# Optimization experiments

Hardware: AMD Instinct MI355X
Metric: run time of the kernel (lower is better)

## Reference

```python
import jax, jax.numpy as jnp
import numpy as np

DIM = 256; SEQ = 2048; WIN = 64; HEADS = 4; RANK = 32; LAYERS = 3; VOCAB = 32000
EPS = 1e-6

def _unit(v):
    # unit_normalize_values: project onto unit sphere along feature dim
    return v / jnp.maximum(jnp.linalg.norm(v, axis=-1, keepdims=True), EPS)

def _signed_softmax(s):
    # signed_softmax_state: sign(s) * softmax(|s|) over nodes
    return jnp.sign(s) * jax.nn.softmax(jnp.abs(s), axis=-1)

def setup_inputs() -> dict:
    key = jax.random.key(0)
    ks = jax.random.split(key, 10)
    d = DIM
    return {
        "input_ids": jax.random.randint(ks[0], (2, SEQ), 0, VOCAB, dtype=jnp.int32),
        "emb": 0.02 * jax.random.normal(ks[1], (VOCAB, d), jnp.float32),
        "pos_emb": 0.02 * jax.random.normal(ks[2], (SEQ, d), jnp.float32),
        "anchor_val": 0.02 * jax.random.normal(ks[3], (d,), jnp.float32),
        "anchor_state": jnp.zeros((), jnp.float32),
        "Ws": 0.02 * jax.random.normal(ks[4], (d,), jnp.float32),
        "bs": jnp.zeros((), jnp.float32),
        "U": 0.02 * jax.random.normal(ks[5], (LAYERS, d, HEADS, RANK), jnp.float32),
        "V": 0.02 * jax.random.normal(ks[6], (LAYERS, d, HEADS, RANK), jnp.float32),
        "W1": 0.02 * jax.random.normal(ks[7], (LAYERS, d, 2 * d), jnp.float32),
        "b1": jnp.zeros((LAYERS, 2 * d), jnp.float32),
        "W2": 0.02 * jax.random.normal(ks[8], (LAYERS, 2 * d, d), jnp.float32),
        "b2": jnp.zeros((LAYERS, d), jnp.float32),
    }

def _forward(emb, pos_emb, anchor_val, anchor_state, Ws, bs, U, V, W1, b1, W2, b2, input_ids):
    B, S = input_ids.shape
    tok = emb[input_ids] + pos_emb[None, :S]          # [B,S,D]
    state_src = tok                                    # state projected from pre-unit-norm values
    tok = _unit(tok)
    tstate = state_src @ Ws + bs                       # [B,S] scalar state per node
    val = jnp.concatenate([jnp.broadcast_to(_unit(anchor_val), (B, 1, DIM)), tok], axis=1)
    state = jnp.concatenate([jnp.broadcast_to(anchor_state, (B, 1)), tstate], axis=1)
    N = S + 1
    offs = jnp.arange(-WIN, WIN + 1)
    idx = jnp.arange(N)[:, None] + offs[None, :]       # [N,K]
    valid = (idx >= 0) & (idx < N)
    idxc = jnp.clip(idx, 0, N - 1)
    inv_sqrt_r = np.float32(1.0 / np.sqrt(RANK))
    for l in range(LAYERS):
        q = jnp.einsum('bnd,dhr->bnhr', val, U[l])
        k = jnp.einsum('bnd,dhr->bnhr', val, V[l])
        knb = k[:, idxc]                               # [B,N,K,H,R] window gather
        s = jnp.einsum('bnhr,bnkhr->bnkh', q, knb) * inv_sqrt_r
        s = s.max(axis=-1)                             # max head-aggregate [B,N,K]
        a = jnp.where(valid, jnp.abs(s), -jnp.inf)
        wgt = jnp.where(valid, jnp.sign(s) * jax.nn.softmax(a, axis=-1), 0.0)  # signed-abs-softmax edges
        dval = jnp.einsum('bnk,bnkd->bnd', wgt, val[:, idxc])
        dstate = jnp.sum(wgt * state[:, idxc], axis=-1)
        # apply_delta: residual + norm(identity) + unit-norm + touched-mask where
        updated = val + dval
        nv = _unit(updated)
        touched = jnp.max(jnp.abs(jax.lax.stop_gradient(dval)), axis=-1, keepdims=True) > 0
        val = jnp.where(touched, nv, updated)
        state = _signed_softmax(state + dstate)
        # residual feed-forward then re-unit-norm
        h = jax.nn.gelu(jnp.einsum('bnd,dh->bnh', val, W1[l]) + b1[l], approximate=False)
        val = _unit(val + jnp.einsum('bnh,hd->bnd', h, W2[l]) + b2[l])
    return state, val

def reference(input_ids, emb, pos_emb, anchor_val, anchor_state, Ws, bs, U, V, W1, b1, W2, b2):
    return _forward(emb, pos_emb, anchor_val, anchor_state, Ws, bs, U, V, W1, b1, W2, b2, input_ids)
```

## Files before the change

kernel.cpp:

```cpp
#include <hip/hip_runtime.h>
#include <hip/hip_bf16.h>
#include <math.h>

#define BB 2
#define SS 2048
#define NN 2049
#define MM (BB*NN)
#define DD 256
#define HR 128
#define NHEAD 4
#define WINW 64
#define DFF 512
#define EPSF 1e-6f
#define TB8 257

typedef __attribute__((ext_vector_type(8))) short bf16x8;
typedef __attribute__((ext_vector_type(4))) float f32x4;

__device__ __forceinline__ float wave_sum(float v) {
    v += __shfl_down(v, 32, 64); v += __shfl_down(v, 16, 64);
    v += __shfl_down(v, 8, 64);  v += __shfl_down(v, 4, 64);
    v += __shfl_down(v, 2, 64);  v += __shfl_down(v, 1, 64);
    return v;
}
__device__ __forceinline__ float wave_max(float v) {
    v = fmaxf(v, __shfl_down(v, 32, 64)); v = fmaxf(v, __shfl_down(v, 16, 64));
    v = fmaxf(v, __shfl_down(v, 8, 64));  v = fmaxf(v, __shfl_down(v, 4, 64));
    v = fmaxf(v, __shfl_down(v, 2, 64));  v = fmaxf(v, __shfl_down(v, 1, 64));
    return v;
}
__device__ __forceinline__ float block_sum(float v, float* red) {
    v = wave_sum(v);
    __syncthreads();
    if ((threadIdx.x & 63) == 0) red[threadIdx.x >> 6] = v;
    __syncthreads();
    return red[0] + red[1] + red[2] + red[3];
}
__device__ __forceinline__ float sgnf(float x) {
    return (x > 0.f) ? 1.f : ((x < 0.f) ? -1.f : 0.f);
}
__device__ __forceinline__ ushort f2b(float x) {
    __hip_bfloat16 h = __float2bfloat16(x);
    return *(ushort*)&h;
}
__device__ __forceinline__ float b2f(ushort u) {
    unsigned int v = ((unsigned int)u) << 16;
    return *(float*)&v;
}
__device__ __forceinline__ void split3(float x, ushort& h, ushort& m, ushort& l) {
    h = f2b(x);
    float r1 = x - b2f(h);
    m = f2b(r1);
    l = f2b(r1 - b2f(m));
}
__device__ __forceinline__ void pack_map(int e, int N, int& k, int& n) {
    int j = e & 7;
    int l = (e >> 3) & 63;
    int c = e >> 9;
    int ntiles = N >> 4;
    int kt = c / ntiles, nt = c - kt * ntiles;
    k = kt * 32 + ((l >> 4) << 3) + j;
    n = nt * 16 + (l & 15);
}

__global__ void pre_kernel(const int* __restrict__ ids,
                           const float* __restrict__ emb,
                           const float* __restrict__ pos,
                           const float* __restrict__ anchor_val,
                           const float* __restrict__ anchor_state,
                           const float* __restrict__ Ws,
                           const float* __restrict__ bs,
                           float* __restrict__ val,
                           float* __restrict__ state,
                           const float* __restrict__ W1, const float* __restrict__ W2,
                           const float* __restrict__ U,  const float* __restrict__ V,
                           ushort* __restrict__ W1ph, ushort* __restrict__ W1pl,
                           ushort* __restrict__ W2ph, ushort* __restrict__ W2pl,
                           ushort* __restrict__ U0, ushort* __restrict__ U1,
                           ushort* __restrict__ U2,
                           ushort* __restrict__ V0, ushort* __restrict__ V1,
                           ushort* __restrict__ V2) {
    __shared__ float red[4];
    int bid = blockIdx.x;
    int t = threadIdx.x;
    if (bid < MM) {
        int b = bid / NN, n = bid % NN;
        float e;
        if (n == 0) {
            e = anchor_val[t];
        } else {
            int id = ids[b * SS + (n - 1)];
            e = emb[(size_t)id * DD + t] + pos[(size_t)(n - 1) * DD + t];
        }
        float ss = block_sum(e * e, red);
        float ts = block_sum(e * Ws[t], red);
        float rn = 1.f / fmaxf(sqrtf(ss), EPSF);
        float o = e * rn;
        val[(size_t)bid * DD + t] = o;
        if (t == 0) state[bid] = (n == 0) ? anchor_state[0] : (ts + bs[0]);
        return;
    }
    int idx = (bid - MM) * 256 + t;
    int l = idx / 327680;
    int r = idx - l * 327680;
    if (l >= 3) return;
    int k, n;
    if (r < 131072) {
        int e = r;
        pack_map(e, 512, k, n);
        float s = W1[(size_t)l * 131072 + (size_t)k * 512 + n];
        ushort h = f2b(s);
        W1ph[(size_t)l * 131072 + e] = h;
        W1pl[(size_t)l * 131072 + e] = f2b(s - b2f(h));
    } else if (r < 262144) {
        int e = r - 131072;
        pack_map(e, 256, k, n);
        float s = W2[(size_t)l * 131072 + (size_t)k * 256 + n];
        ushort h = f2b(s);
        W2ph[(size_t)l * 131072 + e] = h;
        W2pl[(size_t)l * 131072 + e] = f2b(s - b2f(h));
    } else if (r < 294912) {
        int e = r - 262144;
        pack_map(e, 128, k, n);
        ushort h, m, lo;
        split3(U[(size_t)l * 32768 + (size_t)k * 128 + n], h, m, lo);
        U0[(size_t)l * 32768 + e] = h;
        U1[(size_t)l * 32768 + e] = m;
        U2[(size_t)l * 32768 + e] = lo;
    } else {
        int e = r - 294912;
        pack_map(e, 128, k, n);
        ushort h, m, lo;
        split3(V[(size_t)l * 32768 + (size_t)k * 128 + n], h, m, lo);
        V0[(size_t)l * 32768 + e] = h;
        V1[(size_t)l * 32768 + e] = m;
        V2[(size_t)l * 32768 + e] = lo;
    }
}

__global__ __launch_bounds__(256, 3)
void proj_kernel(const float* __restrict__ Xin,
                 const ushort* __restrict__ U0, const ushort* __restrict__ U1,
                 const ushort* __restrict__ U2,
                 const ushort* __restrict__ V0, const ushort* __restrict__ V1,
                 const ushort* __restrict__ V2,
                 ushort* __restrict__ q0, ushort* __restrict__ q1,
                 ushort* __restrict__ q2,
                 ushort* __restrict__ k0, ushort* __restrict__ k1,
                 ushort* __restrict__ k2,
                 float* __restrict__ valG, int donorm) {
    __shared__ __align__(16) ushort pln[3][16 * 256];
    int t = threadIdx.x;
    int w = t >> 6, l = t & 63;
    int lm = l & 15, quad = l >> 4;
    int m0 = blockIdx.x * 16;
    bool isQ = (blockIdx.y == 0);
    const ushort* P0 = isQ ? U0 : V0;
    const ushort* P1 = isQ ? U1 : V1;
    const ushort* P2 = isQ ? U2 : V2;

    #pragma unroll
    for (int rr = 0; rr < 4; rr++) {
        int row = w * 4 + rr;
        int tok = m0 + row; if (tok > MM - 1) tok = MM - 1;
        f32x4 x = *(const f32x4*)(Xin + (size_t)tok * DD + l * 4);
        if (donorm) {
            float s = x[0]*x[0] + x[1]*x[1] + x[2]*x[2] + x[3]*x[3];
            #pragma unroll
            for (int off = 1; off < 64; off <<= 1) s += __shfl_xor(s, off, 64);
            float rn = 1.f / fmaxf(sqrtf(s), EPSF);
            x[0] *= rn; x[1] *= rn; x[2] *= rn; x[3] *= rn;
            if (isQ) *(f32x4*)(valG + (size_t)tok * DD + l * 4) = x;
        }
        ushort4 h4, m4, l4;
        ushort hh, mm, ll;
        split3(x[0], hh, mm, ll); h4.x = hh; m4.x = mm; l4.x = ll;
        split3(x[1], hh, mm, ll); h4.y = hh; m4.y = mm; l4.y = ll;
        split3(x[2], hh, mm, ll); h4.z = hh; m4.z = mm; l4.z = ll;
        split3(x[3], hh, mm, ll); h4.w = hh; m4.w = mm; l4.w = ll;
        unsigned byte = ((unsigned)(row * 512 + l * 8)) ^ ((unsigned)((row & 7) << 4));
        *(ushort4*)((char*)&pln[0][0] + byte) = h4;
        *(ushort4*)((char*)&pln[1][0] + byte) = m4;
        *(ushort4*)((char*)&pln[2][0] + byte) = l4;
    }
    __syncthreads();

    f32x4 acc[2];
    acc[0] = (f32x4)(0.f); acc[1] = (f32x4)(0.f);
    #pragma unroll
    for (int kt = 0; kt < 8; kt++) {
        unsigned abyte = ((unsigned)(lm * 512 + kt * 64 + quad * 16)) ^
                         ((unsigned)((lm & 7) << 4));
        bf16x8 a0 = *(const bf16x8*)((char*)&pln[0][0] + abyte);
        bf16x8 a1 = *(const bf16x8*)((char*)&pln[1][0] + abyte);
        bf16x8 a2 = *(const bf16x8*)((char*)&pln[2][0] + abyte);
        #pragma unroll
        for (int jj = 0; jj < 2; jj++) {
            int ntl = w * 2 + jj;
            size_t off = ((size_t)(kt * 8 + ntl) * 64 + l) * 8;
            bf16x8 b0 = *(const bf16x8*)(P0 + off);
            bf16x8 b1 = *(const bf16x8*)(P1 + off);
            bf16x8 b2 = *(const bf16x8*)(P2 + off);
            acc[jj] = __builtin_amdgcn_mfma_f32_16x16x32_bf16(a0, b0, acc[jj], 0, 0, 0);
            acc[jj] = __builtin_amdgcn_mfma_f32_16x16x32_bf16(a0, b1, acc[jj], 0, 0, 0);
            acc[jj] = __builtin_amdgcn_mfma_f32_16x16x32_bf16(a1, b0, acc[jj], 0, 0, 0);
            acc[jj] = __builtin_amdgcn_mfma_f32_16x16x32_bf16(a1, b1, acc[jj], 0, 0, 0);
            acc[jj] = __builtin_amdgcn_mfma_f32_16x16x32_bf16(a0, b2, acc[jj], 0, 0, 0);
            acc[jj] = __builtin_amdgcn_mfma_f32_16x16x32_bf16(a2, b0, acc[jj], 0, 0, 0);
        }
    }
    ushort* o0 = isQ ? q0 : k0;
    ushort* o1 = isQ ? q1 : k1;
    ushort* o2 = isQ ? q2 : k2;
    #pragma unroll
    for (int jj = 0; jj < 2; jj++) {
        int n = (w * 2 + jj) * 16 + lm;
        #pragma unroll
        for (int r = 0; r < 4; r++) {
            int tok = m0 + quad * 4 + r;
            if (tok < MM) {
                ushort h, m, lo;
                split3(acc[jj][r], h, m, lo);
                size_t oi = (size_t)tok * HR + n;
                o0[oi] = h; o1[oi] = m; o2[oi] = lo;
            }
        }
    }
}

__global__ __launch_bounds__(256, 3)
void attn_kernel(const float* __restrict__ val_in,
                 const float* __restrict__ state_in,
                 const ushort* __restrict__ q0, const ushort* __restrict__ q1,
                 const ushort* __restrict__ q2,
                 const ushort* __restrict__ k0, const ushort* __restrict__ k1,
                 const ushort* __restrict__ k2,
                 float* __restrict__ val_out,
                 ushort* __restrict__ vbH, ushort* __restrict__ vbM,
                 float* __restrict__ dstate_out) {
    __shared__ float sc4[NHEAD][8][148];
    __shared__ float wgt2[144][12];
    __shared__ float redS[8][4];
    __shared__ float redM[8][4];

    int b = blockIdx.x / TB8;
    int n0 = (blockIdx.x % TB8) * 8;
    int t = threadIdx.x;
    int w = t >> 6, l = t & 63;
    int lm = l & 15, quad = l >> 4;

    {
        int qrow = n0 + (lm & 7);
        if (qrow > NN - 1) qrow = NN - 1;
        size_t qa = ((size_t)(b * NN + qrow)) * HR + w * 32 + quad * 8;
        bf16x8 a0 = *(const bf16x8*)(q0 + qa);
        bf16x8 a1 = *(const bf16x8*)(q1 + qa);
        bf16x8 a2 = *(const bf16x8*)(q2 + qa);
        #pragma unroll
        for (int jt = 0; jt < 9; jt++) {
            int j = n0 - 64 + jt * 16 + lm;
            j = (j < 0) ? 0 : ((j > NN - 1) ? NN - 1 : j);
            size_t ka = ((size_t)(b * NN + j)) * HR + w * 32 + quad * 8;
            bf16x8 kf0 = *(const bf16x8*)(k0 + ka);
            bf16x8 kf1 = *(const bf16x8*)(k1 + ka);
            bf16x8 kf2 = *(const bf16x8*)(k2 + ka);
            f32x4 acc = (f32x4)(0.f);
            acc = __builtin_amdgcn_mfma_f32_16x16x32_bf16(a0, kf0, acc, 0, 0, 0);
            acc = __builtin_amdgcn_mfma_f32_16x16x32_bf16(a0, kf1, acc, 0, 0, 0);
            acc = __builtin_amdgcn_mfma_f32_16x16x32_bf16(a1, kf0, acc, 0, 0, 0);
            acc = __builtin_amdgcn_mfma_f32_16x16x32_bf16(a1, kf1, acc, 0, 0, 0);
            acc = __builtin_amdgcn_mfma_f32_16x16x32_bf16(a0, kf2, acc, 0, 0, 0);
            acc = __builtin_amdgcn_mfma_f32_16x16x32_bf16(a2, kf0, acc, 0, 0, 0);
            if (quad < 2) {
                #pragma unroll
                for (int r = 0; r < 4; r++)
                    sc4[w][quad * 4 + r][jt * 16 + lm] = acc[r];
            }
        }
    }
    __syncthreads();

    {
        int m = t >> 5, p = t & 31;
        int n = n0 + m;
        bool tokv = (n < NN);
        float sv[5]; bool vv[5];
        float mx = -INFINITY;
        #pragma unroll
        for (int i = 0; i < 5; i++) {
            int tap = p + 32 * i;
            bool inb = (tap < 144);
            int tapc = inb ? tap : 0;
            int j = n0 - 64 + tapc;
            float s0 = sc4[0][m][tapc], s1 = sc4[1][m][tapc];
            float s2 = sc4[2][m][tapc], s3 = sc4[3][m][tapc];
            float s = fmaxf(fmaxf(s0, s1), fmaxf(s2, s3)) * 0.17677669529663687f;
            bool v = inb && tokv && (tap >= m) && (tap <= m + 128) && (j >= 0) && (j < NN);
            sv[i] = s; vv[i] = v;
            if (v) mx = fmaxf(mx, fabsf(s));
        }
        for (int off = 16; off > 0; off >>= 1) mx = fmaxf(mx, __shfl_xor(mx, off, 64));
        float ee[5];
        float sum = 0.f;
        #pragma unroll
        for (int i = 0; i < 5; i++) {
            ee[i] = vv[i] ? expf(fabsf(sv[i]) - mx) : 0.f;
            sum += ee[i];
        }
        for (int off = 16; off > 0; off >>= 1) sum += __shfl_xor(sum, off, 64);
        float inv = (sum > 0.f) ? 1.f / sum : 0.f;
        float ds = 0.f;
        #pragma unroll
        for (int i = 0; i < 5; i++) {
            int tap = p + 32 * i;
            if (tap < 144) {
                float wg = vv[i] ? sgnf(sv[i]) * ee[i] * inv : 0.f;
                wgt2[tap][m] = wg;
                if (vv[i]) ds += wg * state_in[b * NN + (n0 - 64 + tap)];
            }
        }
        for (int off = 16; off > 0; off >>= 1) ds += __shfl_xor(ds, off, 64);
        if (p == 0 && tokv) dstate_out[b * NN + n] = ds;
    }
    __syncthreads();

    {
        int d = (t >> 2) * 4;
        int tg = t & 3;
        int tok0 = tg * 2, tok1 = tg * 2 + 1;
        int jlo = (n0 >= 64) ? 0 : (64 - n0);
        int jhi = NN - 1 - n0 + 64; if (jhi > 135) jhi = 135;
        const float* vbase = val_in + ((size_t)(b * NN + n0 - 64)) * DD + d;
        f32x4 acc0 = (f32x4)(0.f), acc1 = (f32x4)(0.f);
        int jj = jlo;
        for (; jj + 3 <= jhi; jj += 4) {
            f32x4 v0 = *(const f32x4*)(vbase + (size_t)(jj + 0) * DD);
            f32x4 v1 = *(const f32x4*)(vbase + (size_t)(jj + 1) * DD);
            f32x4 v2 = *(const f32x4*)(vbase + (size_t)(jj + 2) * DD);
            f32x4 v3 = *(const f32x4*)(vbase + (size_t)(jj + 3) * DD);
            float wa0 = wgt2[jj + 0][tok0], wa1 = wgt2[jj + 0][tok1];
            float wb0 = wgt2[jj + 1][tok0], wb1 = wgt2[jj + 1][tok1];
            float wc0 = wgt2[jj + 2][tok0], wc1 = wgt2[jj + 2][tok1];
            float wd0 = wgt2[jj + 3][tok0], wd1 = wgt2[jj + 3][tok1];
            #pragma unroll
            for (int c = 0; c < 4; c++) {
                acc0[c] += v0[c] * wa0 + v1[c] * wb0 + v2[c] * wc0 + v3[c] * wd0;
                acc1[c] += v0[c] * wa1 + v1[c] * wb1 + v2[c] * wc1 + v3[c] * wd1;
            }
        }
        for (; jj <= jhi; jj++) {
            f32x4 v = *(const f32x4*)(vbase + (size_t)jj * DD);
            float w0 = wgt2[jj][tok0], w1 = wgt2[jj][tok1];
            #pragma unroll
            for (int c = 0; c < 4; c++) {
                acc0[c] += v[c] * w0;
                acc1[c] += v[c] * w1;
            }
        }
        f32x4 u[2]; f32x4 ac[2]; ac[0] = acc0; ac[1] = acc1;
        #pragma unroll
        for (int ti = 0; ti < 2; ti++) {
            int tok = tg * 2 + ti;
            int n = n0 + tok;
            f32x4 vold = (f32x4)(0.f);
            if (n < NN) vold = *(const f32x4*)(val_in + ((size_t)(b * NN + n)) * DD + d);
            u[ti] = vold + ac[ti];
            float s = u[ti][0]*u[ti][0] + u[ti][1]*u[ti][1] + u[ti][2]*u[ti][2] + u[ti][3]*u[ti][3];
            float mb = fmaxf(fmaxf(fabsf(ac[ti][0]), fabsf(ac[ti][1])),
                             fmaxf(fabsf(ac[ti][2]), fabsf(ac[ti][3])));
            for (int off = 4; off <= 32; off <<= 1) {
                s += __shfl_xor(s, off, 64);
                mb = fmaxf(mb, __shfl_xor(mb, off, 64));
            }
            if ((l >> 2) == 0) { redS[tok][w] = s; redM[tok][w] = mb; }
        }
        __syncthreads();
        #pragma unroll
        for (int ti = 0; ti < 2; ti++) {
            int tok = tg * 2 + ti;
            int n = n0 + tok;
            if (n < NN) {
                float ss = redS[tok][0] + redS[tok][1] + redS[tok][2] + redS[tok][3];
                float mab = fmaxf(fmaxf(redM[tok][0], redM[tok][1]),
                                  fmaxf(redM[tok][2], redM[tok][3]));
                float rn = 1.f / fmaxf(sqrtf(ss), EPSF);
                f32x4 o = u[ti];
                if (mab > 0.f) { o[0] *= rn; o[1] *= rn; o[2] *= rn; o[3] *= rn; }
                size_t oi = ((size_t)(b * NN + n)) * DD + d;
                *(f32x4*)(val_out + oi) = o;
                ushort4 hv, mv;
                {
                    ushort h0 = f2b(o[0]); hv.x = h0; mv.x = f2b(o[0] - b2f(h0));
                    ushort h1 = f2b(o[1]); hv.y = h1; mv.y = f2b(o[1] - b2f(h1));
                    ushort h2 = f2b(o[2]); hv.z = h2; mv.z = f2b(o[2] - b2f(h2));
                    ushort h3 = f2b(o[3]); hv.w = h3; mv.w = f2b(o[3] - b2f(h3));
                }
                *(ushort4*)(vbH + oi) = hv;
                *(ushort4*)(vbM + oi) = mv;
            }
        }
    }
}

__global__ __launch_bounds__(256, 3)
void ffn1_kernel(const ushort* __restrict__ XbH, const ushort* __restrict__ XbM,
                 const ushort* __restrict__ W1h, const ushort* __restrict__ W1l,
                 const float*  __restrict__ b1,
                 ushort* __restrict__ Hh, ushort* __restrict__ Hl,
                 const float* __restrict__ state_in, const float* __restrict__ dstate,
                 float* __restrict__ state_out) {
    __shared__ float red[8];
    int t = threadIdx.x;

    if (blockIdx.x == 257) {
        int b = blockIdx.y;
        float lmax = -INFINITY;
        for (int n = t; n < NN; n += 256) {
            float x = state_in[b * NN + n] + dstate[b * NN + n];
            lmax = fmaxf(lmax, fabsf(x));
        }
        lmax = wave_max(lmax);
        if ((t & 63) == 0) red[t >> 6] = lmax;
        __syncthreads();
        float m = fmaxf(fmaxf(red[0], red[1]), fmaxf(red[2], red[3]));
        float lsum = 0.f;
        for (int n = t; n < NN; n += 256)
            lsum += expf(fabsf(state_in[b * NN + n] + dstate[b * NN + n]) - m);
        lsum = wave_sum(lsum);
        __syncthreads();
        if ((t & 63) == 0) red[4 + (t >> 6)] = lsum;
        __syncthreads();
        float inv = 1.f / (red[4] + red[5] + red[6] + red[7]);
        for (int n = t; n < NN; n += 256) {
            float x = state_in[b * NN + n] + dstate[b * NN + n];
            state_out[b * NN + n] = sgnf(x) * expf(fabsf(x) - m) * inv;
        }
        return;
    }

    int w = t >> 6, l = t & 63;
    int lm = l & 15, quad = l >> 4;
    int m0 = blockIdx.x * 16;
    int nh = blockIdx.y;
    int row0 = m0 + lm; if (row0 > MM - 1) row0 = MM - 1;
    const ushort* xh = XbH + (size_t)row0 * DD + quad * 8;
    const ushort* xm = XbM + (size_t)row0 * DD + quad * 8;

    f32x4 acc[4];
    #pragma unroll
    for (int jj = 0; jj < 4; jj++) acc[jj] = (f32x4)(0.f);

    #pragma unroll
    for (int kt = 0; kt < 8; kt++) {
        bf16x8 ah = *(const bf16x8*)(xh + kt * 32);
        bf16x8 am = *(const bf16x8*)(xm + kt * 32);
        #pragma unroll
        for (int jj = 0; jj < 4; jj++) {
            int ntl = w * 4 + jj;
            size_t off = ((size_t)(kt * 32 + nh * 16 + ntl) * 64 + l) * 8;
            bf16x8 bh = *(const bf16x8*)(W1h + off);
            bf16x8 bl = *(const bf16x8*)(W1l + off);
            acc[jj] = __builtin_amdgcn_mfma_f32_16x16x32_bf16(ah, bh, acc[jj], 0, 0, 0);
            acc[jj] = __builtin_amdgcn_mfma_f32_16x16x32_bf16(am, bh, acc[jj], 0, 0, 0);
            acc[jj] = __builtin_amdgcn_mfma_f32_16x16x32_bf16(ah, bl, acc[jj], 0, 0, 0);
        }
    }
    #pragma unroll
    for (int jj = 0; jj < 4; jj++) {
        int gn = nh * 256 + (w * 4 + jj) * 16 + lm;
        float bb = b1[gn];
        #pragma unroll
        for (int r = 0; r < 4; r++) {
            int tok = m0 + quad * 4 + r;
            if (tok < MM) {
                float x = acc[jj][r] + bb;
                float g = 0.5f * x * (1.f + erff(x * 0.70710678118654752f));
                ushort gh = f2b(g);
                size_t oi = (size_t)tok * DFF + gn;
                Hh[oi] = gh;
                Hl[oi] = f2b(g - b2f(gh));
            }
        }
    }
}

__global__ __launch_bounds__(256, 4)
void ffn2_kernel(const ushort* __restrict__ Hh, const ushort* __restrict__ Hl,
                 const float*  __restrict__ Xf,
                 const ushort* __restrict__ W2h, const ushort* __restrict__ W2l,
                 const float*  __restrict__ b2,
                 float* __restrict__ Yb) {
    int t = threadIdx.x;
    int w = t >> 6, l = t & 63;
    int lm = l & 15, quad = l >> 4;
    int m0 = blockIdx.x * 16;
    int nh = blockIdx.y;
    int row0 = m0 + lm; if (row0 > MM - 1) row0 = MM - 1;
    const ushort* xh = Hh + (size_t)row0 * DFF + quad * 8;
    const ushort* xl = Hl + (size_t)row0 * DFF + quad * 8;

    f32x4 acc[2];
    acc[0] = (f32x4)(0.f); acc[1] = (f32x4)(0.f);

    #pragma unroll
    for (int kt = 0; kt < 16; kt++) {
        bf16x8 ah = *(const bf16x8*)(xh + kt * 32);
        bf16x8 al = *(const bf16x8*)(xl + kt * 32);
        #pragma unroll
        for (int jj = 0; jj < 2; jj++) {
            int ntl = w * 2 + jj;
            size_t off = ((size_t)(kt * 16 + nh * 8 + ntl) * 64 + l) * 8;
            bf16x8 bh = *(const bf16x8*)(W2h + off);
            bf16x8 bl = *(const bf16x8*)(W2l + off);
            acc[jj] = __builtin_amdgcn_mfma_f32_16x16x32_bf16(ah, bh, acc[jj], 0, 0, 0);
            acc[jj] = __builtin_amdgcn_mfma_f32_16x16x32_bf16(al, bh, acc[jj], 0, 0, 0);
            acc[jj] = __builtin_amdgcn_mfma_f32_16x16x32_bf16(ah, bl, acc[jj], 0, 0, 0);
        }
    }
    #pragma unroll
    for (int jj = 0; jj < 2; jj++) {
        int gn = nh * 128 + (w * 2 + jj) * 16 + lm;
        float bb = b2[gn];
        #pragma unroll
        for (int r = 0; r < 4; r++) {
            int tok = m0 + quad * 4 + r;
            if (tok < MM) {
                size_t oi = (size_t)tok * DD + gn;
                Yb[oi] = Xf[oi] + acc[jj][r] + bb;
            }
        }
    }
}

__global__ void ffn3f_kernel(const float* __restrict__ Yb,
                             float* __restrict__ val_out) {
    int t = threadIdx.x;
    int w = t >> 6, l = t & 63;
    int row = blockIdx.x * 4 + w;
    if (row >= MM) return;
    f32x4 y = *(const f32x4*)(Yb + (size_t)row * DD + l * 4);
    float s = y[0]*y[0] + y[1]*y[1] + y[2]*y[2] + y[3]*y[3];
    #pragma unroll
    for (int off = 1; off < 64; off <<= 1) s += __shfl_xor(s, off, 64);
    float rn = 1.f / fmaxf(sqrtf(s), EPSF);
    f32x4 o;
    o[0] = y[0] * rn; o[1] = y[1] * rn; o[2] = y[2] * rn; o[3] = y[3] * rn;
    *(f32x4*)(val_out + (size_t)row * DD + l * 4) = o;
}

extern "C" void kernel_launch(void* const* d_in, const int* in_sizes, int n_in,
                              void* d_out, int out_size, void* d_ws, size_t ws_size,
                              hipStream_t stream) {
    const int*   ids          = (const int*)d_in[0];
    const float* emb          = (const float*)d_in[1];
    const float* pos          = (const float*)d_in[2];
    const float* anchor_val   = (const float*)d_in[3];
    const float* anchor_state = (const float*)d_in[4];
    const float* Ws           = (const float*)d_in[5];
    const float* bs           = (const float*)d_in[6];
    const float* U            = (const float*)d_in[7];
    const float* V            = (const float*)d_in[8];
    const float* W1           = (const float*)d_in[9];
    const float* b1           = (const float*)d_in[10];
    const float* W2           = (const float*)d_in[11];
    const float* b2           = (const float*)d_in[12];
    float* out = (float*)d_out;

    ushort* p = (ushort*)d_ws;
    ushort* vB0 = p; p += (size_t)MM * DD;
    ushort* vB1 = p; p += (size_t)MM * DD;
    ushort* q0b = p; p += (size_t)MM * HR;
    ushort* q1b = p; p += (size_t)MM * HR;
    ushort* q2b = p; p += (size_t)MM * HR;
    ushort* k0b = p; p += (size_t)MM * HR;
    ushort* k1b = p; p += (size_t)MM * HR;
    ushort* k2b = p; p += (size_t)MM * HR;
    ushort* Hh  = p; p += (size_t)MM * DFF;
    ushort* Hl  = p; p += (size_t)MM * DFF;
    ushort* W1ph = p; p += 3 * 131072;
    ushort* W1pl = p; p += 3 * 131072;
    ushort* W2ph = p; p += 3 * 131072;
    ushort* W2pl = p; p += 3 * 131072;
    ushort* U0p = p; p += 3 * 32768;
    ushort* U1p = p; p += 3 * 32768;
    ushort* U2p = p; p += 3 * 32768;
    ushort* V0p = p; p += 3 * 32768;
    ushort* V1p = p; p += 3 * 32768;
    ushort* V2p = p; p += 3 * 32768;
    float* f = (float*)p;
    float* valA = f; f += (size_t)MM * DD;
    float* valB = f; f += (size_t)MM * DD;
    float* Yb   = f; f += (size_t)MM * DD;
    float* st0  = f; f += MM;
    float* st1  = f; f += MM;
    float* dst  = f; f += MM;

    pre_kernel<<<MM + 3840, 256, 0, stream>>>(ids, emb, pos, anchor_val, anchor_state,
                                              Ws, bs, valA, st0,
                                              W1, W2, U, V,
                                              W1ph, W1pl, W2ph, W2pl,
                                              U0p, U1p, U2p, V0p, V1p, V2p);
    float* s_in = st0;
    float* s_out = st1;
    for (int l = 0; l < 3; l++) {
        const float* Xin = (l == 0) ? valA : Yb;
        proj_kernel<<<dim3(257, 2), 256, 0, stream>>>(
            Xin,
            U0p + (size_t)l * 32768, U1p + (size_t)l * 32768, U2p + (size_t)l * 32768,
            V0p + (size_t)l * 32768, V1p + (size_t)l * 32768, V2p + (size_t)l * 32768,
            q0b, q1b, q2b, k0b, k1b, k2b,
            valA, (l == 0) ? 0 : 1);
        attn_kernel<<<BB * TB8, 256, 0, stream>>>(valA, s_in,
                                                  q0b, q1b, q2b, k0b, k1b, k2b,
                                                  valB, vB0, vB1, dst);
        ffn1_kernel<<<dim3(258, 2), 256, 0, stream>>>(
            vB0, vB1,
            W1ph + (size_t)l * 131072, W1pl + (size_t)l * 131072, b1 + (size_t)l * DFF,
            Hh, Hl,
            s_in, dst, (l == 2) ? out : s_out);
        ffn2_kernel<<<dim3(257, 2), 256, 0, stream>>>(
            Hh, Hl, valB,
            W2ph + (size_t)l * 131072, W2pl + (size_t)l * 131072, b2 + (size_t)l * DD,
            Yb);
        float* tmp = s_in; s_in = s_out; s_out = tmp;
    }
    ffn3f_kernel<<<(MM + 3) / 4, 256, 0, stream>>>(Yb, out + MM);
}
```

Measured before the change: 360.0 us.

## Fuse all layer stages into one cooperative persistent kernel with grid syncs

Turns the separate pre, projection, attention, FFN and normalisation kernels into device functions. It then runs them all from a single cooperative mega-kernel of 514 blocks that loops over jobs and uses grid.sync between stages. The goal is to remove the per-kernel launch overhead and tail gaps across the many small launches for three layers. The trade-off is that every stage now shares one launch configuration and shared-memory size, which may lower occupancy or per-stage efficiency. The original multi-kernel path stays as a fallback if the cooperative launch fails.

```diff
diff --git a/kernel.cpp b/kernel.cpp
--- a/kernel.cpp
+++ b/kernel.cpp
@@ -1,6 +1,9 @@
 #include <hip/hip_runtime.h>
+#include <hip/hip_cooperative_groups.h>
 #include <hip/hip_bf16.h>
 #include <math.h>
+
+namespace cg = cooperative_groups;
 
 #define BB 2
 #define SS 2048
@@ -13,6 +16,7 @@
 #define DFF 512
 #define EPSF 1e-6f
 #define TB8 257
+#define SMEM_BYTES 26112
 
 typedef __attribute__((ext_vector_type(8))) short bf16x8;
 typedef __attribute__((ext_vector_type(4))) float f32x4;
@@ -63,44 +67,36 @@
     n = nt * 16 + (l & 15);
 }
 
-__global__ void pre_kernel(const int* __restrict__ ids,
-                           const float* __restrict__ emb,
-                           const float* __restrict__ pos,
-                           const float* __restrict__ anchor_val,
-                           const float* __restrict__ anchor_state,
-                           const float* __restrict__ Ws,
-                           const float* __restrict__ bs,
-                           float* __restrict__ val,
-                           float* __restrict__ state,
-                           const float* __restrict__ W1, const float* __restrict__ W2,
-                           const float* __restrict__ U,  const float* __restrict__ V,
-                           ushort* __restrict__ W1ph, ushort* __restrict__ W1pl,
-                           ushort* __restrict__ W2ph, ushort* __restrict__ W2pl,
-                           ushort* __restrict__ U0, ushort* __restrict__ U1,
-                           ushort* __restrict__ U2,
-                           ushort* __restrict__ V0, ushort* __restrict__ V1,
-                           ushort* __restrict__ V2) {
-    __shared__ float red[4];
-    int bid = blockIdx.x;
-    int t = threadIdx.x;
-    if (bid < MM) {
-        int b = bid / NN, n = bid % NN;
-        float e;
-        if (n == 0) {
-            e = anchor_val[t];
-        } else {
-            int id = ids[b * SS + (n - 1)];
-            e = emb[(size_t)id * DD + t] + pos[(size_t)(n - 1) * DD + t];
-        }
-        float ss = block_sum(e * e, red);
-        float ts = block_sum(e * Ws[t], red);
-        float rn = 1.f / fmaxf(sqrtf(ss), EPSF);
-        float o = e * rn;
-        val[(size_t)bid * DD + t] = o;
-        if (t == 0) state[bid] = (n == 0) ? anchor_state[0] : (ts + bs[0]);
-        return;
-    }
-    int idx = (bid - MM) * 256 + t;
+
+__device__ __forceinline__ void embed_job(int row, int t, float* red,
+    const int* __restrict__ ids, const float* __restrict__ emb,
+    const float* __restrict__ pos, const float* __restrict__ anchor_val,
+    const float* __restrict__ anchor_state, const float* __restrict__ Ws,
+    const float* __restrict__ bs, float* __restrict__ val, float* __restrict__ state)
+{
+    int b = row / NN, n = row % NN;
+    float e;
+    if (n == 0) {
+        e = anchor_val[t];
+    } else {
+        int id = ids[b * SS + (n - 1)];
+        e = emb[(size_t)id * DD + t] + pos[(size_t)(n - 1) * DD + t];
+    }
+    float ss = block_sum(e * e, red);
+    float ts = block_sum(e * Ws[t], red);
+    float rn = 1.f / fmaxf(sqrtf(ss), EPSF);
+    val[(size_t)row * DD + t] = e * rn;
+    if (t == 0) state[row] = (n == 0) ? anchor_state[0] : (ts + bs[0]);
+}
+
+__device__ __forceinline__ void pack_job(int idx,
+    const float* __restrict__ W1, const float* __restrict__ W2,
+    const float* __restrict__ U,  const float* __restrict__ V,
+    ushort* __restrict__ W1ph, ushort* __restrict__ W1pl,
+    ushort* __restrict__ W2ph, ushort* __restrict__ W2pl,
+    ushort* __restrict__ U0, ushort* __restrict__ U1, ushort* __restrict__ U2,
+    ushort* __restrict__ V0, ushort* __restrict__ V1, ushort* __restrict__ V2)
+{
     int l = idx / 327680;
     int r = idx - l * 327680;
     if (l >= 3) return;
@@ -138,26 +134,15 @@
     }
 }
 
-__global__ __launch_bounds__(256, 3)
-void proj_kernel(const float* __restrict__ Xin,
-                 const ushort* __restrict__ U0, const ushort* __restrict__ U1,
-                 const ushort* __restrict__ U2,
-                 const ushort* __restrict__ V0, const ushort* __restrict__ V1,
-                 const ushort* __restrict__ V2,
-                 ushort* __restrict__ q0, ushort* __restrict__ q1,
-                 ushort* __restrict__ q2,
-                 ushort* __restrict__ k0, ushort* __restrict__ k1,
-                 ushort* __restrict__ k2,
-                 float* __restrict__ valG, int donorm) {
-    __shared__ __align__(16) ushort pln[3][16 * 256];
-    int t = threadIdx.x;
+__device__ __forceinline__ void proj_tile(int m0, int donorm, int writeVal,
+    const float* __restrict__ Xin,
+    const ushort* __restrict__ P0, const ushort* __restrict__ P1,
+    const ushort* __restrict__ P2,
+    ushort* __restrict__ o0, ushort* __restrict__ o1, ushort* __restrict__ o2,
+    float* __restrict__ valG, char* smem, int t)
+{
     int w = t >> 6, l = t & 63;
     int lm = l & 15, quad = l >> 4;
-    int m0 = blockIdx.x * 16;
-    bool isQ = (blockIdx.y == 0);
-    const ushort* P0 = isQ ? U0 : V0;
-    const ushort* P1 = isQ ? U1 : V1;
-    const ushort* P2 = isQ ? U2 : V2;
 
     #pragma unroll
     for (int rr = 0; rr < 4; rr++) {
@@ -170,7 +155,7 @@
             for (int off = 1; off < 64; off <<= 1) s += __shfl_xor(s, off, 64);
             float rn = 1.f / fmaxf(sqrtf(s), EPSF);
             x[0] *= rn; x[1] *= rn; x[2] *= rn; x[3] *= rn;
-            if (isQ) *(f32x4*)(valG + (size_t)tok * DD + l * 4) = x;
+            if (writeVal) *(f32x4*)(valG + (size_t)tok * DD + l * 4) = x;
         }
         ushort4 h4, m4, l4;
         ushort hh, mm, ll;
@@ -179,9 +164,9 @@
         split3(x[2], hh, mm, ll); h4.z = hh; m4.z = mm; l4.z = ll;
         split3(x[3], hh, mm, ll); h4.w = hh; m4.w = mm; l4.w = ll;
         unsigned byte = ((unsigned)(row * 512 + l * 8)) ^ ((unsigned)((row & 7) << 4));
-        *(ushort4*)((char*)&pln[0][0] + byte) = h4;
-        *(ushort4*)((char*)&pln[1][0] + byte) = m4;
-        *(ushort4*)((char*)&pln[2][0] + byte) = l4;
+        *(ushort4*)(smem + 0 * 8192 + byte) = h4;
+        *(ushort4*)(smem + 1 * 8192 + byte) = m4;
+        *(ushort4*)(smem + 2 * 8192 + byte) = l4;
     }
     __syncthreads();
 
@@ -191,9 +176,9 @@
     for (int kt = 0; kt < 8; kt++) {
         unsigned abyte = ((unsigned)(lm * 512 + kt * 64 + quad * 16)) ^
                          ((unsigned)((lm & 7) << 4));
-        bf16x8 a0 = *(const bf16x8*)((char*)&pln[0][0] + abyte);
-        bf16x8 a1 = *(const bf16x8*)((char*)&pln[1][0] + abyte);
-        bf16x8 a2 = *(const bf16x8*)((char*)&pln[2][0] + abyte);
+        bf16x8 a0 = *(const bf16x8*)(smem + 0 * 8192 + abyte);
+        bf16x8 a1 = *(const bf16x8*)(smem + 1 * 8192 + abyte);
+        bf16x8 a2 = *(const bf16x8*)(smem + 2 * 8192 + abyte);
         #pragma unroll
         for (int jj = 0; jj < 2; jj++) {
             int ntl = w * 2 + jj;
@@ -209,9 +194,6 @@
             acc[jj] = __builtin_amdgcn_mfma_f32_16x16x32_bf16(a2, b0, acc[jj], 0, 0, 0);
         }
     }
-    ushort* o0 = isQ ? q0 : k0;
-    ushort* o1 = isQ ? q1 : k1;
-    ushort* o2 = isQ ? q2 : k2;
     #pragma unroll
     for (int jj = 0; jj < 2; jj++) {
         int n = (w * 2 + jj) * 16 + lm;
@@ -226,26 +208,23 @@
             }
         }
     }
-}
-
-__global__ __launch_bounds__(256, 3)
-void attn_kernel(const float* __restrict__ val_in,
-                 const float* __restrict__ state_in,
-                 const ushort* __restrict__ q0, const ushort* __restrict__ q1,
-                 const ushort* __restrict__ q2,
-                 const ushort* __restrict__ k0, const ushort* __restrict__ k1,
-                 const ushort* __restrict__ k2,
-                 float* __restrict__ val_out,
-                 ushort* __restrict__ vbH, ushort* __restrict__ vbM,
-                 float* __restrict__ dstate_out) {
-    __shared__ float sc4[NHEAD][8][148];
-    __shared__ float wgt2[144][12];
-    __shared__ float redS[8][4];
-    __shared__ float redM[8][4];
-
-    int b = blockIdx.x / TB8;
-    int n0 = (blockIdx.x % TB8) * 8;
-    int t = threadIdx.x;
+    __syncthreads();
+}
+
+__device__ __forceinline__ void attn_tile(int b, int n0, int t, char* smem,
+    const float* __restrict__ val_in, const float* __restrict__ state_in,
+    const ushort* __restrict__ q0, const ushort* __restrict__ q1,
+    const ushort* __restrict__ q2,
+    const ushort* __restrict__ k0, const ushort* __restrict__ k1,
+    const ushort* __restrict__ k2,
+    float* __restrict__ val_out,
+    ushort* __restrict__ vbH, ushort* __restrict__ vbM,
+    float* __restrict__ dstate_out)
+{
+    float* sc4  = (float*)smem;
+    float* wgt2 = (float*)(smem + 18944);
+    float* redS = (float*)(smem + 25856);
+    float* redM = (float*)(smem + 25984);
     int w = t >> 6, l = t & 63;
     int lm = l & 15, quad = l >> 4;
 
@@ -274,7 +253,7 @@
             if (quad < 2) {
                 #pragma unroll
                 for (int r = 0; r < 4; r++)
-                    sc4[w][quad * 4 + r][jt * 16 + lm] = acc[r];
+                    sc4[((size_t)w * 8 + quad * 4 + r) * 148 + jt * 16 + lm] = acc[r];
             }
         }
     }
@@ -292,8 +271,8 @@
             bool inb = (tap < 144);
             int tapc = inb ? tap : 0;
             int j = n0 - 64 + tapc;
-            float s0 = sc4[0][m][tapc], s1 = sc4[1][m][tapc];
-            float s2 = sc4[2][m][tapc], s3 = sc4[3][m][tapc];
+            float s0 = sc4[(0 * 8 + m) * 148 + tapc], s1 = sc4[(1 * 8 + m) * 148 + tapc];
+            float s2 = sc4[(2 * 8 + m) * 148 + tapc], s3 = sc4[(3 * 8 + m) * 148 + tapc];
             float s = fmaxf(fmaxf(s0, s1), fmaxf(s2, s3)) * 0.17677669529663687f;
             bool v = inb && tokv && (tap >= m) && (tap <= m + 128) && (j >= 0) && (j < NN);
             sv[i] = s; vv[i] = v;
@@ -315,7 +294,7 @@
             int tap = p + 32 * i;
             if (tap < 144) {
                 float wg = vv[i] ? sgnf(sv[i]) * ee[i] * inv : 0.f;
-                wgt2[tap][m] = wg;
+                wgt2[tap * 12 + m] = wg;
                 if (vv[i]) ds += wg * state_in[b * NN + (n0 - 64 + tap)];
             }
         }
@@ -338,10 +317,10 @@
             f32x4 v1 = *(const f32x4*)(vbase + (size_t)(jj + 1) * DD);
             f32x4 v2 = *(const f32x4*)(vbase + (size_t)(jj + 2) * DD);
             f32x4 v3 = *(const f32x4*)(vbase + (size_t)(jj + 3) * DD);
-            float wa0 = wgt2[jj + 0][tok0], wa1 = wgt2[jj + 0][tok1];
-            float wb0 = wgt2[jj + 1][tok0], wb1 = wgt2[jj + 1][tok1];
-            float wc0 = wgt2[jj + 2][tok0], wc1 = wgt2[jj + 2][tok1];
-            float wd0 = wgt2[jj + 3][tok0], wd1 = wgt2[jj + 3][tok1];
+            float wa0 = wgt2[(jj + 0) * 12 + tok0], wa1 = wgt2[(jj + 0) * 12 + tok1];
+            float wb0 = wgt2[(jj + 1) * 12 + tok0], wb1 = wgt2[(jj + 1) * 12 + tok1];
+            float wc0 = wgt2[(jj + 2) * 12 + tok0], wc1 = wgt2[(jj + 2) * 12 + tok1];
+            float wd0 = wgt2[(jj + 3) * 12 + tok0], wd1 = wgt2[(jj + 3) * 12 + tok1];
             #pragma unroll
             for (int c = 0; c < 4; c++) {
                 acc0[c] += v0[c] * wa0 + v1[c] * wb0 + v2[c] * wc0 + v3[c] * wd0;
@@ -350,7 +329,7 @@
         }
         for (; jj <= jhi; jj++) {
             f32x4 v = *(const f32x4*)(vbase + (size_t)jj * DD);
-            float w0 = wgt2[jj][tok0], w1 = wgt2[jj][tok1];
+            float w0 = wgt2[jj * 12 + tok0], w1 = wgt2[jj * 12 + tok1];
             #pragma unroll
             for (int c = 0; c < 4; c++) {
                 acc0[c] += v[c] * w0;
@@ -372,7 +351,7 @@
                 s += __shfl_xor(s, off, 64);
                 mb = fmaxf(mb, __shfl_xor(mb, off, 64));
             }
-            if ((l >> 2) == 0) { redS[tok][w] = s; redM[tok][w] = mb; }
+            if ((l >> 2) == 0) { redS[tok * 4 + w] = s; redM[tok * 4 + w] = mb; }
         }
         __syncthreads();
         #pragma unroll
@@ -380,9 +359,9 @@
             int tok = tg * 2 + ti;
             int n = n0 + tok;
             if (n < NN) {
-                float ss = redS[tok][0] + redS[tok][1] + redS[tok][2] + redS[tok][3];
-                float mab = fmaxf(fmaxf(redM[tok][0], redM[tok][1]),
-                                  fmaxf(redM[tok][2], redM[tok][3]));
+                float ss = redS[tok * 4 + 0] + redS[tok * 4 + 1] + redS[tok * 4 + 2] + redS[tok * 4 + 3];
+                float mab = fmaxf(fmaxf(redM[tok * 4 + 0], redM[tok * 4 + 1]),
+                                  fmaxf(redM[tok * 4 + 2], redM[tok * 4 + 3]));
                 float rn = 1.f / fmaxf(sqrtf(ss), EPSF);
                 f32x4 o = u[ti];
                 if (mab > 0.f) { o[0] *= rn; o[1] *= rn; o[2] *= rn; o[3] *= rn; }
@@ -400,48 +379,17 @@
             }
         }
     }
-}
-
-__global__ __launch_bounds__(256, 3)
-void ffn1_kernel(const ushort* __restrict__ XbH, const ushort* __restrict__ XbM,
-                 const ushort* __restrict__ W1h, const ushort* __restrict__ W1l,
-                 const float*  __restrict__ b1,
-                 ushort* __restrict__ Hh, ushort* __restrict__ Hl,
-                 const float* __restrict__ state_in, const float* __restrict__ dstate,
-                 float* __restrict__ state_out) {
-    __shared__ float red[8];
-    int t = threadIdx.x;
-
-    if (blockIdx.x == 257) {
-        int b = blockIdx.y;
-        float lmax = -INFINITY;
-        for (int n = t; n < NN; n += 256) {
-            float x = state_in[b * NN + n] + dstate[b * NN + n];
-            lmax = fmaxf(lmax, fabsf(x));
-        }
-        lmax = wave_max(lmax);
-        if ((t & 63) == 0) red[t >> 6] = lmax;
-        __syncthreads();
-        float m = fmaxf(fmaxf(red[0], red[1]), fmaxf(red[2], red[3]));
-        float lsum = 0.f;
-        for (int n = t; n < NN; n += 256)
-            lsum += expf(fabsf(state_in[b * NN + n] + dstate[b * NN + n]) - m);
-        lsum = wave_sum(lsum);
-        __syncthreads();
-        if ((t & 63) == 0) red[4 + (t >> 6)] = lsum;
-        __syncthreads();
-        float inv = 1.f / (red[4] + red[5] + red[6] + red[7]);
-        for (int n = t; n < NN; n += 256) {
-            float x = state_in[b * NN + n] + dstate[b * NN + n];
-            state_out[b * NN + n] = sgnf(x) * expf(fabsf(x) - m) * inv;
-        }
-        return;
-    }
-
+    __syncthreads();
+}
+
+__device__ __forceinline__ void ffn1_tile(int m0, int nh, int t,
+    const ushort* __restrict__ XbH, const ushort* __restrict__ XbM,
+    const ushort* __restrict__ W1h, const ushort* __restrict__ W1l,
+    const float* __restrict__ b1,
+    ushort* __restrict__ Hh, ushort* __restrict__ Hl)
+{
     int w = t >> 6, l = t & 63;
     int lm = l & 15, quad = l >> 4;
-    int m0 = blockIdx.x * 16;
-    int nh = blockIdx.y;
     int row0 = m0 + lm; if (row0 > MM - 1) row0 = MM - 1;
     const ushort* xh = XbH + (size_t)row0 * DD + quad * 8;
     const ushort* xm = XbM + (size_t)row0 * DD + quad * 8;
@@ -484,17 +432,42 @@
     }
 }
 
-__global__ __launch_bounds__(256, 4)
-void ffn2_kernel(const ushort* __restrict__ Hh, const ushort* __restrict__ Hl,
-                 const float*  __restrict__ Xf,
-                 const ushort* __restrict__ W2h, const ushort* __restrict__ W2l,
-                 const float*  __restrict__ b2,
-                 float* __restrict__ Yb) {
-    int t = threadIdx.x;
+__device__ __forceinline__ void state_job(int b, int t, float* red,
+    const float* __restrict__ state_in, const float* __restrict__ dstate,
+    float* __restrict__ state_out)
+{
+    float lmax = -INFINITY;
+    for (int n = t; n < NN; n += 256) {
+        float x = state_in[b * NN + n] + dstate[b * NN + n];
+        lmax = fmaxf(lmax, fabsf(x));
+    }
+    lmax = wave_max(lmax);
+    if ((t & 63) == 0) red[t >> 6] = lmax;
+    __syncthreads();
+    float m = fmaxf(fmaxf(red[0], red[1]), fmaxf(red[2], red[3]));
+    float lsum = 0.f;
+    for (int n = t; n < NN; n += 256)
+        lsum += expf(fabsf(state_in[b * NN + n] + dstate[b * NN + n]) - m);
+    lsum = wave_sum(lsum);
+    __syncthreads();
+    if ((t & 63) == 0) red[4 + (t >> 6)] = lsum;
+    __syncthreads();
+    float inv = 1.f / (red[4] + red[5] + red[6] + red[7]);
+    for (int n = t; n < NN; n += 256) {
+        float x = state_in[b * NN + n] + dstate[b * NN + n];
+        state_out[b * NN + n] = sgnf(x) * expf(fabsf(x) - m) * inv;
+    }
+    __syncthreads();
+}
+
+__device__ __forceinline__ void ffn2_tile(int m0, int nh, int t,
+    const ushort* __restrict__ Hh, const ushort* __restrict__ Hl,
+    const float* __restrict__ Xf,
+    const ushort* __restrict__ W2h, const ushort* __restrict__ W2l,
+    const float* __restrict__ b2, float* __restrict__ Yb)
+{
     int w = t >> 6, l = t & 63;
     int lm = l & 15, quad = l >> 4;
-    int m0 = blockIdx.x * 16;
-    int nh = blockIdx.y;
     int row0 = m0 + lm; if (row0 > MM - 1) row0 = MM - 1;
     const ushort* xh = Hh + (size_t)row0 * DFF + quad * 8;
     const ushort* xl = Hl + (size_t)row0 * DFF + quad * 8;
@@ -532,11 +505,11 @@
     }
 }
 
-__global__ void ffn3f_kernel(const float* __restrict__ Yb,
-                             float* __restrict__ val_out) {
-    int t = threadIdx.x;
+__device__ __forceinline__ void norm_row4(int job, int t,
+    const float* __restrict__ Yb, float* __restrict__ val_out)
+{
     int w = t >> 6, l = t & 63;
-    int row = blockIdx.x * 4 + w;
+    int row = job * 4 + w;
     if (row >= MM) return;
     f32x4 y = *(const f32x4*)(Yb + (size_t)row * DD + l * 4);
     float s = y[0]*y[0] + y[1]*y[1] + y[2]*y[2] + y[3]*y[3];
@@ -547,6 +520,197 @@
     o[0] = y[0] * rn; o[1] = y[1] * rn; o[2] = y[2] * rn; o[3] = y[3] * rn;
     *(f32x4*)(val_out + (size_t)row * DD + l * 4) = o;
 }
+
+
+__global__ __launch_bounds__(256, 3)
+void mega_kernel(const int* __restrict__ ids, const float* __restrict__ emb,
+                 const float* __restrict__ pos, const float* __restrict__ anchor_val,
+                 const float* __restrict__ anchor_state, const float* __restrict__ Ws,
+                 const float* __restrict__ bs, const float* __restrict__ U,
+                 const float* __restrict__ V, const float* __restrict__ W1,
+                 const float* __restrict__ b1, const float* __restrict__ W2,
+                 const float* __restrict__ b2, void* __restrict__ ws,
+                 float* __restrict__ out)
+{
+    __shared__ __align__(16) char smem[SMEM_BYTES];
+    cg::grid_group grid = cg::this_grid();
+    int t = threadIdx.x;
+
+    ushort* p = (ushort*)ws;
+    ushort* vB0 = p; p += (size_t)MM * DD;
+    ushort* vB1 = p; p += (size_t)MM * DD;
+    ushort* q0b = p; p += (size_t)MM * HR;
+    ushort* q1b = p; p += (size_t)MM * HR;
+    ushort* q2b = p; p += (size_t)MM * HR;
+    ushort* k0b = p; p += (size_t)MM * HR;
+    ushort* k1b = p; p += (size_t)MM * HR;
+    ushort* k2b = p; p += (size_t)MM * HR;
+    ushort* Hh  = p; p += (size_t)MM * DFF;
+    ushort* Hl  = p; p += (size_t)MM * DFF;
+    ushort* W1ph = p; p += 3 * 131072;
+    ushort* W1pl = p; p += 3 * 131072;
+    ushort* W2ph = p; p += 3 * 131072;
+    ushort* W2pl = p; p += 3 * 131072;
+    ushort* U0p = p; p += 3 * 32768;
+    ushort* U1p = p; p += 3 * 32768;
+    ushort* U2p = p; p += 3 * 32768;
+    ushort* V0p = p; p += 3 * 32768;
+    ushort* V1p = p; p += 3 * 32768;
+    ushort* V2p = p; p += 3 * 32768;
+    float* f = (float*)p;
+    float* valA = f; f += (size_t)MM * DD;
+    float* valB = f; f += (size_t)MM * DD;
+    float* Yb   = f; f += (size_t)MM * DD;
+    float* st0  = f; f += MM;
+    float* st1  = f; f += MM;
+    float* dst  = f; f += MM;
+
+    for (int job = blockIdx.x; job < MM + 3840; job += gridDim.x) {
+        if (job < MM)
+            embed_job(job, t, (float*)smem, ids, emb, pos, anchor_val, anchor_state,
+                      Ws, bs, valA, st0);
+        else
+            pack_job((job - MM) * 256 + t, W1, W2, U, V,
+                     W1ph, W1pl, W2ph, W2pl, U0p, U1p, U2p, V0p, V1p, V2p);
+    }
+    grid.sync();
+
+    float* s_in = st0;
+    float* s_out = st1;
+    #pragma unroll 1
+    for (int l = 0; l < 3; l++) {
+        const ushort* U0l = U0p + (size_t)l * 32768;
+        const ushort* U1l = U1p + (size_t)l * 32768;
+        const ushort* U2l = U2p + (size_t)l * 32768;
+        const ushort* V0l = V0p + (size_t)l * 32768;
+        const ushort* V1l = V1p + (size_t)l * 32768;
+        const ushort* V2l = V2p + (size_t)l * 32768;
+        const ushort* W1hl = W1ph + (size_t)l * 131072;
+        const ushort* W1ll = W1pl + (size_t)l * 131072;
+        const ushort* W2hl = W2ph + (size_t)l * 131072;
+        const ushort* W2ll = W2pl + (size_t)l * 131072;
+        const float* b1l = b1 + (size_t)l * DFF;
+        const float* b2l = b2 + (size_t)l * DD;
+        const float* Xin = (l == 0) ? valA : Yb;
+        int donorm = (l == 0) ? 0 : 1;
+        float* stTgt = (l == 2) ? out : s_out;
+
+        for (int job = blockIdx.x; job < 514; job += gridDim.x) {
+            int xb = job % 257;
+            bool isQ = (job < 257);
+            proj_tile(xb * 16, donorm, donorm && isQ, Xin,
+                      isQ ? U0l : V0l, isQ ? U1l : V1l, isQ ? U2l : V2l,
+                      isQ ? q0b : k0b, isQ ? q1b : k1b, isQ ? q2b : k2b,
+                      valA, smem, t);
+        }
+        grid.sync();
+
+        for (int job = blockIdx.x; job < 514; job += gridDim.x)
+            attn_tile(job / 257, (job % 257) * 8, t, smem, valA, s_in,
+                      q0b, q1b, q2b, k0b, k1b, k2b, valB, vB0, vB1, dst);
+        grid.sync();
+
+        for (int job = blockIdx.x; job < 514; job += gridDim.x)
+            ffn1_tile((job % 257) * 16, job / 257, t, vB0, vB1, W1hl, W1ll, b1l, Hh, Hl);
+        grid.sync();
+
+        for (int job = blockIdx.x; job < 516; job += gridDim.x) {
+            if (job < 514)
+                ffn2_tile((job % 257) * 16, job / 257, t, Hh, Hl, valB, W2hl, W2ll, b2l, Yb);
+            else
+                state_job(job - 514, t, (float*)smem, s_in, dst, stTgt);
+        }
+        grid.sync();
+
+        float* tmp = s_in; s_in = s_out; s_out = tmp;
+    }
+
+    for (int job = blockIdx.x; job < 1025; job += gridDim.x)
+        norm_row4(job, t, Yb, out + MM);
+}
+
+
+__global__ void pre_kernel(const int* __restrict__ ids, const float* __restrict__ emb,
+                           const float* __restrict__ pos, const float* __restrict__ anchor_val,
+                           const float* __restrict__ anchor_state, const float* __restrict__ Ws,
+                           const float* __restrict__ bs, float* __restrict__ val,
+                           float* __restrict__ state,
+                           const float* __restrict__ W1, const float* __restrict__ W2,
+                           const float* __restrict__ U,  const float* __restrict__ V,
+                           ushort* W1ph, ushort* W1pl, ushort* W2ph, ushort* W2pl,
+                           ushort* U0, ushort* U1, ushort* U2,
+                           ushort* V0, ushort* V1, ushort* V2) {
+    __shared__ float red[4];
+    int bid = blockIdx.x;
+    int t = threadIdx.x;
+    if (bid < MM) {
+        embed_job(bid, t, red, ids, emb, pos, anchor_val, anchor_state, Ws, bs, val, state);
+        return;
+    }
+    pack_job((bid - MM) * 256 + t, W1, W2, U, V,
+             W1ph, W1pl, W2ph, W2pl, U0, U1, U2, V0, V1, V2);
+}
+
+__global__ __launch_bounds__(256, 3)
+void proj_kernel(const float* __restrict__ Xin,
+                 const ushort* __restrict__ U0, const ushort* __restrict__ U1,
+                 const ushort* __restrict__ U2,
+                 const ushort* __restrict__ V0, const ushort* __restrict__ V1,
+                 const ushort* __restrict__ V2,
+                 ushort* __restrict__ q0, ushort* __restrict__ q1,
+                 ushort* __restrict__ q2,
+                 ushort* __restrict__ k0, ushort* __restrict__ k1,
+                 ushort* __restrict__ k2,
+                 float* __restrict__ valG, int donorm) {
+    __shared__ __align__(16) char smem[SMEM_BYTES];
+    bool isQ = (blockIdx.y == 0);
+    proj_tile(blockIdx.x * 16, donorm, donorm && isQ, Xin,
+              isQ ? U0 : V0, isQ ? U1 : V1, isQ ? U2 : V2,
+              isQ ? q0 : k0, isQ ? q1 : k1, isQ ? q2 : k2,
+              valG, smem, threadIdx.x);
+}
+
+__global__ __launch_bounds__(256, 3)
+void attn_kernel(const float* __restrict__ val_in, const float* __restrict__ state_in,
+                 const ushort* __restrict__ q0, const ushort* __restrict__ q1,
+                 const ushort* __restrict__ q2,
+                 const ushort* __restrict__ k0, const ushort* __restrict__ k1,
+                 const ushort* __restrict__ k2,
+                 float* __restrict__ val_out,
+                 ushort* __restrict__ vbH, ushort* __restrict__ vbM,
+                 float* __restrict__ dstate_out) {
+    __shared__ __align__(16) char smem[SMEM_BYTES];
+    attn_tile(blockIdx.x / TB8, (blockIdx.x % TB8) * 8, threadIdx.x, smem,
+              val_in, state_in, q0, q1, q2, k0, k1, k2, val_out, vbH, vbM, dstate_out);
+}
+
+__global__ __launch_bounds__(256, 3)
+void ffn1_kernel(const ushort* __restrict__ XbH, const ushort* __restrict__ XbM,
+                 const ushort* __restrict__ W1h, const ushort* __restrict__ W1l,
+                 const float*  __restrict__ b1,
+                 ushort* __restrict__ Hh, ushort* __restrict__ Hl,
+                 const float* __restrict__ state_in, const float* __restrict__ dstate,
+                 float* __restrict__ state_out) {
+    __shared__ float red[8];
+    if (blockIdx.x == 257) {
+        state_job(blockIdx.y, threadIdx.x, red, state_in, dstate, state_out);
+        return;
+    }
+    ffn1_tile(blockIdx.x * 16, blockIdx.y, threadIdx.x, XbH, XbM, W1h, W1l, b1, Hh, Hl);
+}
+
+__global__ __launch_bounds__(256, 4)
+void ffn2_kernel(const ushort* __restrict__ Hh, const ushort* __restrict__ Hl,
+                 const float*  __restrict__ Xf,
+                 const ushort* __restrict__ W2h, const ushort* __restrict__ W2l,
+                 const float*  __restrict__ b2, float* __restrict__ Yb) {
+    ffn2_tile(blockIdx.x * 16, blockIdx.y, threadIdx.x, Hh, Hl, Xf, W2h, W2l, b2, Yb);
+}
+
+__global__ void ffn3f_kernel(const float* __restrict__ Yb, float* __restrict__ val_out) {
+    norm_row4(blockIdx.x, threadIdx.x, Yb, val_out);
+}
+
 
 extern "C" void kernel_launch(void* const* d_in, const int* in_sizes, int n_in,
                               void* d_out, int out_size, void* d_ws, size_t ws_size,
@@ -565,6 +729,19 @@
     const float* W2           = (const float*)d_in[11];
     const float* b2           = (const float*)d_in[12];
     float* out = (float*)d_out;
+    void* ws = d_ws;
+
+    {
+        void* args[15] = {
+            (void*)&ids, (void*)&emb, (void*)&pos, (void*)&anchor_val,
+            (void*)&anchor_state, (void*)&Ws, (void*)&bs, (void*)&U, (void*)&V,
+            (void*)&W1, (void*)&b1, (void*)&W2, (void*)&b2, (void*)&ws, (void*)&out
+        };
+        hipError_t err = hipLaunchCooperativeKernel(
+            reinterpret_cast<void*>(mega_kernel), dim3(514), dim3(256), args, 0, stream);
+        if (err == hipSuccess) return;
+        (void)hipGetLastError();
+    }
 
     ushort* p = (ushort*)d_ws;
     ushort* vB0 = p; p += (size_t)MM * DD;
```

After: 1.132 ms. +214.3%, slower.
